# Optimization experiments

Measured on AMD Instinct MI355X. Metric: run time of the kernel, lower is better.

Reference implementation:

```python
import jax, jax.numpy as jnp
import numpy as np

WH, WW = 8, 8
NUM_HEADS = 8
DIM = 256
MLP_HIDDEN = 1024
EPS = 1e-5


def _rel_pos_index(wh, ww):
    ch, cw = np.meshgrid(np.arange(wh), np.arange(ww), indexing='ij')
    flat = np.stack([ch.ravel(), cw.ravel()])            # (2, N)
    rel = flat[:, :, None] - flat[:, None, :]            # (2, N, N)
    rel = rel.transpose(1, 2, 0).copy()                  # (N, N, 2)
    rel[:, :, 0] += wh - 1
    rel[:, :, 1] += ww - 1
    rel[:, :, 0] *= 2 * ww - 1
    return jnp.asarray(rel.sum(-1))                      # (N, N) int

REL_IDX = _rel_pos_index(WH, WW)


def _layernorm(x, g, b):
    mu = x.mean(-1, keepdims=True)
    var = ((x - mu) ** 2).mean(-1, keepdims=True)
    return (x - mu) * jax.lax.rsqrt(var + EPS) * g + b


def _window_partition(x):
    B, H, W, C = x.shape
    x = x.reshape(B, H // WH, WH, W // WW, WW, C)
    return x.transpose(0, 1, 3, 2, 4, 5).reshape(-1, WH * WW, C)


def _window_reverse(w, B, H, W):
    C = w.shape[-1]
    x = w.reshape(B, H // WH, W // WW, WH, WW, C)
    return x.transpose(0, 1, 3, 2, 4, 5).reshape(B, H, W, C)


def _window_attn(qx, kvx, qw, qb, kvw, kvb, bias_table, pw, pb):
    # qx/kvx: [Bw, N, C]; weights stored as [in, out] (torch Linear transposed)
    Bw, N, C = qx.shape
    hd = C // NUM_HEADS
    scale = hd ** -0.5
    q = (qx @ qw + qb).reshape(Bw, N, NUM_HEADS, hd).transpose(0, 2, 1, 3) * scale
    kv = (kvx @ kvw + kvb).reshape(Bw, N, 2, NUM_HEADS, hd)
    k = kv[:, :, 0].transpose(0, 2, 1, 3)
    v = kv[:, :, 1].transpose(0, 2, 1, 3)
    attn = jnp.einsum('bhnd,bhmd->bhnm', q, k)
    bias = bias_table[REL_IDX.reshape(-1)].reshape(N, N, NUM_HEADS).transpose(2, 0, 1)
    attn = jax.nn.softmax(attn + bias[None], axis=-1)
    out = jnp.einsum('bhnm,bhmd->bhnd', attn, v).transpose(0, 2, 1, 3).reshape(Bw, N, C)
    return out @ pw + pb


def setup_inputs() -> dict:
    key = jax.random.key(0)
    ks = jax.random.split(key, 16)
    B, H, W, C = 4, 160, 160, DIM
    nW = (H // WH) * (W // WW)
    N = WH * WW
    n_bias = (2 * WH - 1) * (2 * WW - 1)  # 225
    s = 0.02
    return {
        'x': jax.random.normal(ks[0], (B, H, W, C), jnp.float32),
        'enc_feat': jax.random.normal(ks[1], (B, H, W, C), jnp.float32),
        'mask_matrix': jnp.zeros((nW, N, N), jnp.float32),
        'norm1_g': jnp.ones((C,), jnp.float32),
        'norm1_b': jnp.zeros((C,), jnp.float32),
        'q1_w': jax.random.normal(ks[2], (C, C), jnp.float32) * s,
        'q1_b': jnp.zeros((C,), jnp.float32),
        'kv1_w': jax.random.normal(ks[3], (C, 2 * C), jnp.float32) * s,
        'kv1_b': jnp.zeros((2 * C,), jnp.float32),
        'bias1': jax.random.normal(ks[4], (n_bias, NUM_HEADS), jnp.float32) * s,
        'proj1_w': jax.random.normal(ks[5], (C, C), jnp.float32) * s,
        'proj1_b': jnp.zeros((C,), jnp.float32),
        'q2_w': jax.random.normal(ks[6], (C, C), jnp.float32) * s,
        'q2_b': jnp.zeros((C,), jnp.float32),
        'kv2_w': jax.random.normal(ks[7], (C, 2 * C), jnp.float32) * s,
        'kv2_b': jnp.zeros((2 * C,), jnp.float32),
        'bias2': jax.random.normal(ks[8], (n_bias, NUM_HEADS), jnp.float32) * s,
        'proj2_w': jax.random.normal(ks[9], (C, C), jnp.float32) * s,
        'proj2_b': jnp.zeros((C,), jnp.float32),
        'norm2_g': jnp.ones((C,), jnp.float32),
        'norm2_b': jnp.zeros((C,), jnp.float32),
        'fc1_w': jax.random.normal(ks[10], (C, MLP_HIDDEN), jnp.float32) * s,
        'fc1_b': jnp.zeros((MLP_HIDDEN,), jnp.float32),
        'fc2_w': jax.random.normal(ks[11], (MLP_HIDDEN, C), jnp.float32) * s,
        'fc2_b': jnp.zeros((C,), jnp.float32),
    }


def reference(x, enc_feat, mask_matrix, norm1_g, norm1_b, q1_w, q1_b, kv1_w, kv1_b,
              bias1, proj1_w, proj1_b, q2_w, q2_b, kv2_w, kv2_b, bias2, proj2_w,
              proj2_b, norm2_g, norm2_b, fc1_w, fc1_b, fc2_w, fc2_b):
    # NOTE: the source forward never passes mask_matrix into attention; faithful here.
    B, H, W, C = x.shape
    shortcut = x
    xn = _layernorm(x, norm1_g, norm1_b)
    xw = _window_partition(xn)              # [B*nW, N, C]
    ew = _window_partition(enc_feat)        # [B*nW, N, C]
    # windowed self-attention with relative position bias
    xw = _window_attn(xw, xw, q1_w, q1_b, kv1_w, kv1_b, bias1, proj1_w, proj1_b)
    # windowed cross-attention to encoder features
    xw = _window_attn(xw, ew, q2_w, q2_b, kv2_w, kv2_b, bias2, proj2_w, proj2_b)
    x = shortcut + _window_reverse(xw, B, H, W)
    h = _layernorm(x, norm2_g, norm2_b)
    h = jax.nn.gelu(h @ fc1_w + fc1_b, approximate=False) @ fc2_w + fc2_b
    return x + h
```

## Files before the change

### kernel.cpp

```cpp
#include <hip/hip_runtime.h>

typedef __attribute__((ext_vector_type(4))) float f32x4;
typedef __attribute__((ext_vector_type(8))) short bf16x8;
typedef __attribute__((ext_vector_type(8))) unsigned short ushort8;
typedef unsigned short u16;
typedef unsigned int u32;

#define LDS_AS(p) ((__attribute__((address_space(3))) void*)(p))
#define GLB_AS(p) ((const __attribute__((address_space(1))) void*)(p))

__device__ __forceinline__ u16 f2b(float f) {
    u32 u = __builtin_bit_cast(u32, f);
    u32 r = (u + 0x7fffu + ((u >> 16) & 1u)) >> 16;
    return (u16)r;
}

__device__ __forceinline__ void vmwait(int n) {
    if (n == 0)
        asm volatile("s_waitcnt vmcnt(0)" ::: "memory");
    else if (n == 4)
        asm volatile("s_waitcnt vmcnt(4)" ::: "memory");
    else if (n == 8)
        asm volatile("s_waitcnt vmcnt(8)" ::: "memory");
    else
        asm volatile("s_waitcnt vmcnt(12)" ::: "memory");
}

struct PrepAll {
    const float* src[8];
    u16* dst[8];
    int K[8];
    int N[8];
    float S[8];
};

__global__ __launch_bounds__(256) void prep_w(PrepAll p) {
    const int wi = blockIdx.y;
    const int K = p.K[wi], N = p.N[wi];
    const int e = blockIdx.x * 256 + threadIdx.x;
    if (e >= K * N) return;
    const int k = e / N, n = e % N;
    p.dst[wi][n * K + k] = f2b(p.src[wi][e] * p.S[wi]);
}

__global__ __launch_bounds__(64) void prep_bias(const float* __restrict__ t1,
                                                const float* __restrict__ t2,
                                                float* __restrict__ Bm) {
    const int j = threadIdx.x;
    const int i = blockIdx.x;
    const int hh = blockIdx.y;
    const int s = hh >> 3, h = hh & 7;
    const int idx = ((i >> 3) - (j >> 3) + 7) * 15 + ((i & 7) - (j & 7) + 7);
    const float* tab = s ? t2 : t1;
    Bm[(long)hh * 4096 + i * 64 + j] = tab[idx * 8 + h];
}

__global__ __launch_bounds__(256) void prep_bcat(const float* __restrict__ q1b,
                                                 const float* __restrict__ kv1b,
                                                 const float* __restrict__ q2b,
                                                 float qs, float* __restrict__ b1cat,
                                                 float* __restrict__ q2bs) {
    const int g = blockIdx.x * 256 + threadIdx.x;
    if (g < 256) {
        b1cat[g] = qs * q1b[g];
        q2bs[g] = qs * q2b[g];
    } else if (g < 768) {
        b1cat[g] = kv1b[g - 256];
    }
}

__global__ __launch_bounds__(256) void cast_bf(const float* __restrict__ in,
                                               u16* __restrict__ out) {
    const long i = (long)blockIdx.x * 256 + threadIdx.x;
    const float4 a = *(const float4*)(in + i * 8);
    const float4 b = *(const float4*)(in + i * 8 + 4);
    ushort8 o;
    o[0] = f2b(a.x); o[1] = f2b(a.y); o[2] = f2b(a.z); o[3] = f2b(a.w);
    o[4] = f2b(b.x); o[5] = f2b(b.y); o[6] = f2b(b.z); o[7] = f2b(b.w);
    *(ushort8*)(out + i * 8) = o;
}

__global__ __launch_bounds__(256) void ln256(const float* __restrict__ x,
                                             const float* __restrict__ g,
                                             const float* __restrict__ b,
                                             u16* __restrict__ out) {
    const int lane = threadIdx.x & 63;
    const long row = (long)blockIdx.x * 4 + (threadIdx.x >> 6);
    const float4 v = *(const float4*)(x + row * 256 + lane * 4);
    float s = v.x + v.y + v.z + v.w;
    float s2 = v.x * v.x + v.y * v.y + v.z * v.z + v.w * v.w;
#pragma unroll
    for (int off = 32; off > 0; off >>= 1) {
        s += __shfl_xor(s, off);
        s2 += __shfl_xor(s2, off);
    }
    const float mu = s * (1.f / 256.f);
    const float var = s2 * (1.f / 256.f) - mu * mu;
    const float rr = rsqrtf(var + 1e-5f);
    const int c = lane * 4;
    const float4 gv = *(const float4*)(g + c);
    const float4 bv = *(const float4*)(b + c);
    ushort4 o;
    o.x = f2b((v.x - mu) * rr * gv.x + bv.x);
    o.y = f2b((v.y - mu) * rr * gv.y + bv.y);
    o.z = f2b((v.z - mu) * rr * gv.z + bv.z);
    o.w = f2b((v.w - mu) * rr * gv.w + bv.w);
    *(ushort4*)(out + row * 256 + c) = o;
}

template <int EPI, int NT>
__global__ __launch_bounds__(256, 2) void gemmQ(const u16* __restrict__ A,
                                                const u16* __restrict__ Bt,
                                                const float* __restrict__ bias,
                                                const float* __restrict__ res,
                                                u16* outb, float* outf,
                                                int N, int Nt) {
    constexpr int K = NT * 32;
    static_assert(NT >= 4, "pipeline needs >= 4 K-tiles");
    __shared__ u16 lds[4][2][128 * 32];
    const int t = threadIdx.x;
    const int lane = t & 63;
    const int wave = t >> 6;
    const int wr = wave >> 1, wc = wave & 1;
    const int l15 = lane & 15, lg = lane >> 4;

    const int per = gridDim.x >> 3;
    const int id2 = (blockIdx.x & 7) * per + (blockIdx.x >> 3);
    const int bm = id2 / Nt, bn = id2 % Nt;
    const long m0 = (long)bm * 128;
    const int n0 = bn * 128;

    const u16* Ag = A + (m0 + (t >> 2)) * K + (t & 3) * 8;
    const u16* Bg = Bt + (long)(n0 + (t >> 2)) * K + (t & 3) * 8;

    auto stage = [&](int tile) {
        const int b = tile & 3;
        const int k0 = tile * 32;
        u16* Al = lds[b][0] + t * 8;
        u16* Bl = lds[b][1] + t * 8;
        __builtin_amdgcn_global_load_lds(GLB_AS(Ag + k0), LDS_AS(Al), 16, 0, 0);
        __builtin_amdgcn_global_load_lds(GLB_AS(Ag + (long)64 * K + k0), LDS_AS(Al + 2048), 16, 0, 0);
        __builtin_amdgcn_global_load_lds(GLB_AS(Bg + k0), LDS_AS(Bl), 16, 0, 0);
        __builtin_amdgcn_global_load_lds(GLB_AS(Bg + (long)64 * K + k0), LDS_AS(Bl + 2048), 16, 0, 0);
    };

    f32x4 acc[4][4];
#pragma unroll
    for (int i = 0; i < 4; i++)
#pragma unroll
        for (int j = 0; j < 4; j++) acc[i][j] = (f32x4){0.f, 0.f, 0.f, 0.f};

    stage(0);
    stage(1);
    stage(2);
    stage(3);

#pragma unroll
    for (int tt = 0; tt < NT; ++tt) {
        const int cur = tt & 3;
        const int rem = NT - 1 - tt;
        vmwait(4 * (rem > 3 ? 3 : rem));
        __builtin_amdgcn_s_barrier();

        bf16x8 af[4], bfr[4];
#pragma unroll
        for (int i = 0; i < 4; i++)
            af[i] = *(const bf16x8*)(lds[cur][0] + (wr * 64 + i * 16 + l15) * 32 + lg * 8);
#pragma unroll
        for (int i = 0; i < 4; i++)
            bfr[i] = *(const bf16x8*)(lds[cur][1] + (wc * 64 + i * 16 + l15) * 32 + lg * 8);
        asm volatile("s_waitcnt lgkmcnt(0)" ::: "memory");
        __builtin_amdgcn_sched_barrier(0);
        __builtin_amdgcn_s_barrier();

        if (tt + 4 < NT) stage(tt + 4);

#pragma unroll
        for (int mi = 0; mi < 4; mi++)
#pragma unroll
            for (int ni = 0; ni < 4; ni++)
                acc[mi][ni] = __builtin_amdgcn_mfma_f32_16x16x32_bf16(af[mi], bfr[ni], acc[mi][ni], 0, 0, 0);
    }

#pragma unroll
    for (int mi = 0; mi < 4; mi++) {
#pragma unroll
        for (int ni = 0; ni < 4; ni++) {
            const int col = n0 + wc * 64 + ni * 16 + l15;
            const float bv = bias[col];
#pragma unroll
            for (int r = 0; r < 4; r++) {
                const long row = m0 + wr * 64 + mi * 16 + lg * 4 + r;
                float v = acc[mi][ni][r] + bv;
                if (EPI == 2) v = 0.5f * v * (1.f + erff(v * 0.70710678118f));
                const long idx = row * N + col;
                if (EPI == 3)
                    outf[idx] = v + res[idx];
                else
                    outb[idx] = f2b(v);
            }
        }
    }
}

__global__ __launch_bounds__(256) void attn64(const u16* __restrict__ Q, int qs,
                                              const u16* __restrict__ KV, int ks,
                                              const float* __restrict__ Bm,
                                              u16* __restrict__ AO) {
    __shared__ u16 Plds[4][64 * 72];
    __shared__ u16 Vt[4][32 * 72];
    const int lane = threadIdx.x & 63, wave = threadIdx.x >> 6;
    const int wh = blockIdx.x * 4 + wave;
    const int w = wh >> 3, h = wh & 7;
    const int b = w / 400, rem = w % 400;
    const int wy = rem / 20, wx = rem % 20;
    const long base_t = (long)b * 25600 + wy * 8 * 160 + wx * 8;
    const int l15 = lane & 15, lg = lane >> 4;

    bf16x8 qf[4], kf[4];
#pragma unroll
    for (int ti = 0; ti < 4; ti++) {
        const int r = ti * 16 + l15;
        const long tt = base_t + (r >> 3) * 160 + (r & 7);
        qf[ti] = *(const bf16x8*)(Q + tt * qs + h * 32 + lg * 8);
        kf[ti] = *(const bf16x8*)(KV + tt * ks + h * 32 + lg * 8);
    }
    const f32x4 zz = (f32x4){0.f, 0.f, 0.f, 0.f};
    f32x4 s[4][4];
#pragma unroll
    for (int ti = 0; ti < 4; ti++)
#pragma unroll
        for (int tj = 0; tj < 4; tj++)
            s[ti][tj] = __builtin_amdgcn_mfma_f32_16x16x32_bf16(qf[ti], kf[tj], zz, 0, 0, 0);

    {
        const long tt = base_t + (lane >> 3) * 160 + (lane & 7);
        const u16* vrow = KV + tt * ks + 256 + h * 32;
#pragma unroll
        for (int cg = 0; cg < 4; cg++) {
            bf16x8 v8 = *(const bf16x8*)(vrow + cg * 8);
#pragma unroll
            for (int j = 0; j < 8; j++) Vt[wave][(cg * 8 + j) * 72 + lane] = (u16)v8[j];
        }
    }

    const float* Bh = Bm + h * 4096;
#pragma unroll
    for (int ti = 0; ti < 4; ti++) {
#pragma unroll
        for (int r = 0; r < 4; r++) {
            const int i = ti * 16 + lg * 4 + r;
            float vv[4];
            float m = -1e30f;
#pragma unroll
            for (int tj = 0; tj < 4; tj++) {
                vv[tj] = s[ti][tj][r] + Bh[i * 64 + tj * 16 + l15];
                m = fmaxf(m, vv[tj]);
            }
#pragma unroll
            for (int off = 1; off < 16; off <<= 1) m = fmaxf(m, __shfl_xor(m, off));
            float sum = 0.f;
#pragma unroll
            for (int tj = 0; tj < 4; tj++) {
                vv[tj] = __expf(vv[tj] - m);
                sum += vv[tj];
            }
#pragma unroll
            for (int off = 1; off < 16; off <<= 1) sum += __shfl_xor(sum, off);
            const float inv = 1.f / sum;
#pragma unroll
            for (int tj = 0; tj < 4; tj++)
                Plds[wave][i * 72 + tj * 16 + l15] = f2b(vv[tj] * inv);
        }
    }

    f32x4 o[4][2];
#pragma unroll
    for (int mi = 0; mi < 4; mi++)
#pragma unroll
        for (int n = 0; n < 2; n++) o[mi][n] = zz;
#pragma unroll
    for (int c = 0; c < 2; c++) {
        bf16x8 vf[2];
#pragma unroll
        for (int n = 0; n < 2; n++)
            vf[n] = *(const bf16x8*)(&Vt[wave][(n * 16 + l15) * 72 + c * 32 + lg * 8]);
#pragma unroll
        for (int mi = 0; mi < 4; mi++) {
            bf16x8 pf = *(const bf16x8*)(&Plds[wave][(mi * 16 + l15) * 72 + c * 32 + lg * 8]);
#pragma unroll
            for (int n = 0; n < 2; n++)
                o[mi][n] = __builtin_amdgcn_mfma_f32_16x16x32_bf16(pf, vf[n], o[mi][n], 0, 0, 0);
        }
    }
#pragma unroll
    for (int mi = 0; mi < 4; mi++) {
#pragma unroll
        for (int n = 0; n < 2; n++) {
#pragma unroll
            for (int r = 0; r < 4; r++) {
                const int i = mi * 16 + lg * 4 + r;
                const long tt = base_t + (i >> 3) * 160 + (i & 7);
                AO[tt * 256 + h * 32 + n * 16 + l15] = f2b(o[mi][n][r]);
            }
        }
    }
}

extern "C" void kernel_launch(void* const* d_in, const int* in_sizes, int n_in,
                              void* d_out, int out_size, void* d_ws, size_t ws_size,
                              hipStream_t stream) {
    const float* x    = (const float*)d_in[0];
    const float* enc  = (const float*)d_in[1];
    const float* n1g  = (const float*)d_in[3];
    const float* n1b  = (const float*)d_in[4];
    const float* q1w  = (const float*)d_in[5];
    const float* q1b  = (const float*)d_in[6];
    const float* kv1w = (const float*)d_in[7];
    const float* kv1b = (const float*)d_in[8];
    const float* bias1 = (const float*)d_in[9];
    const float* p1w  = (const float*)d_in[10];
    const float* p1b  = (const float*)d_in[11];
    const float* q2w  = (const float*)d_in[12];
    const float* q2b  = (const float*)d_in[13];
    const float* kv2w = (const float*)d_in[14];
    const float* kv2b = (const float*)d_in[15];
    const float* bias2 = (const float*)d_in[16];
    const float* p2w  = (const float*)d_in[17];
    const float* p2b  = (const float*)d_in[18];
    const float* n2g  = (const float*)d_in[19];
    const float* n2b  = (const float*)d_in[20];
    const float* f1w  = (const float*)d_in[21];
    const float* f1b  = (const float*)d_in[22];
    const float* f2w  = (const float*)d_in[23];
    const float* f2bias = (const float*)d_in[24];
    float* out = (float*)d_out;

    char* ws = (char*)d_ws;
    size_t off = 0;
    auto alloc = [&](size_t bytes) {
        char* p = ws + off;
        off += (bytes + 255) & ~(size_t)255;
        return p;
    };
    u16* Wt    = (u16*)alloc(1048576 * 2);
    float* Bm  = (float*)alloc(16 * 4096 * 4);
    float* b1c = (float*)alloc(768 * 4);
    float* q2s = (float*)alloc(256 * 4);
    u16* xn    = (u16*)alloc(52428800);
    u16* qb    = (u16*)alloc(52428800);
    u16* kvb   = (u16*)alloc(104857600);
    u16* ao    = (u16*)alloc(52428800);
    u16* encb  = (u16*)alloc(52428800);

    u16* qkv = qb;
    u16* h1  = kvb;

    u16 *q1t = Wt, *p1t = Wt + 196608, *q2t = Wt + 262144,
        *kv2t = Wt + 327680, *p2t = Wt + 458752, *f1t = Wt + 524288, *f2t = Wt + 786432;

    const float qscale = 0.17677669529663687f;

    PrepAll pa;
    pa.src[0] = q1w;  pa.dst[0] = q1t;        pa.K[0] = 256;  pa.N[0] = 256;  pa.S[0] = qscale;
    pa.src[1] = kv1w; pa.dst[1] = Wt + 65536; pa.K[1] = 256;  pa.N[1] = 512;  pa.S[1] = 1.f;
    pa.src[2] = p1w;  pa.dst[2] = p1t;        pa.K[2] = 256;  pa.N[2] = 256;  pa.S[2] = 1.f;
    pa.src[3] = q2w;  pa.dst[3] = q2t;        pa.K[3] = 256;  pa.N[3] = 256;  pa.S[3] = qscale;
    pa.src[4] = kv2w; pa.dst[4] = kv2t;       pa.K[4] = 256;  pa.N[4] = 512;  pa.S[4] = 1.f;
    pa.src[5] = p2w;  pa.dst[5] = p2t;        pa.K[5] = 256;  pa.N[5] = 256;  pa.S[5] = 1.f;
    pa.src[6] = f1w;  pa.dst[6] = f1t;        pa.K[6] = 256;  pa.N[6] = 1024; pa.S[6] = 1.f;
    pa.src[7] = f2w;  pa.dst[7] = f2t;        pa.K[7] = 1024; pa.N[7] = 256;  pa.S[7] = 1.f;
    prep_w<<<dim3(1024, 8), 256, 0, stream>>>(pa);
    prep_bias<<<dim3(64, 16), 64, 0, stream>>>(bias1, bias2, Bm);
    prep_bcat<<<dim3(3), 256, 0, stream>>>(q1b, kv1b, q2b, qscale, b1c, q2s);
    cast_bf<<<dim3(12800), 256, 0, stream>>>(enc, encb);
    ln256<<<dim3(25600), 256, 0, stream>>>(x, n1g, n1b, xn);

    gemmQ<0, 8><<<dim3(4800), 256, 0, stream>>>(xn, q1t, b1c, nullptr, qkv, nullptr, 768, 6);
    attn64<<<dim3(3200), 256, 0, stream>>>(qkv, 768, qkv + 256, 768, Bm, ao);
    gemmQ<0, 8><<<dim3(1600), 256, 0, stream>>>(ao, p1t, p1b, nullptr, xn, nullptr, 256, 2);

    gemmQ<0, 8><<<dim3(1600), 256, 0, stream>>>(xn, q2t, q2s, nullptr, qb, nullptr, 256, 2);
    gemmQ<0, 8><<<dim3(3200), 256, 0, stream>>>(encb, kv2t, kv2b, nullptr, kvb, nullptr, 512, 4);
    attn64<<<dim3(3200), 256, 0, stream>>>(qb, 256, kvb, 512, Bm + 8 * 4096, ao);

    gemmQ<3, 8><<<dim3(1600), 256, 0, stream>>>(ao, p2t, p2b, x, (u16*)nullptr, out, 256, 2);

    ln256<<<dim3(25600), 256, 0, stream>>>(out, n2g, n2b, qb);
    for (int c = 0; c < 2; c++) {
        const u16* xh = qb + (size_t)c * 51200 * 256;
        float* oc = out + (size_t)c * 51200 * 256;
        gemmQ<2, 8><<<dim3(3200), 256, 0, stream>>>(xh, f1t, f1b, nullptr, h1, nullptr, 1024, 8);
        gemmQ<3, 32><<<dim3(800), 256, 0, stream>>>(h1, f2t, f2bias, oc, (u16*)nullptr, oc, 256, 2);
    }
}
```

Baseline: 890.0 us.

## Add weight-stationary GEMM for K=256 projections and fuse residual with LayerNorm

Adds a `bres` GEMM kernel for the K=256 GEMMs (QKV, both proj layers, q2, kv2 and fc1). Each wave keeps its 64-column slice of the weight in registers and streams 256 rows of activations through swizzled, double-buffered LDS; the fc1 version applies GELU in the epilogue. The second projection now writes bf16, and a new `ln_add` kernel does the residual add and the second LayerNorm in one pass. The MLP is no longer split into two chunks, and the elementwise and prep kernels loop over several rows or grid-stride to cut block counts. The aim is to reuse each weight tile across many rows and to remove extra launches and fp32 round trips. In exchange, register pressure goes up, the proj2 output is rounded to bf16 before the residual add, and the full-size hidden buffer now runs past `kvb` into the `ao`/`encb` workspace, which is dead by that point.

```diff
diff --git a/kernel.cpp b/kernel.cpp
--- a/kernel.cpp
+++ b/kernel.cpp
@@ -13,6 +13,9 @@
     u32 u = __builtin_bit_cast(u32, f);
     u32 r = (u + 0x7fffu + ((u >> 16) & 1u)) >> 16;
     return (u16)r;
+}
+__device__ __forceinline__ float b2f(u16 u) {
+    return __builtin_bit_cast(float, (u32)u << 16);
 }
 
 __device__ __forceinline__ void vmwait(int n) {
@@ -37,22 +40,23 @@
 __global__ __launch_bounds__(256) void prep_w(PrepAll p) {
     const int wi = blockIdx.y;
     const int K = p.K[wi], N = p.N[wi];
-    const int e = blockIdx.x * 256 + threadIdx.x;
-    if (e >= K * N) return;
-    const int k = e / N, n = e % N;
-    p.dst[wi][n * K + k] = f2b(p.src[wi][e] * p.S[wi]);
-}
-
-__global__ __launch_bounds__(64) void prep_bias(const float* __restrict__ t1,
-                                                const float* __restrict__ t2,
-                                                float* __restrict__ Bm) {
-    const int j = threadIdx.x;
-    const int i = blockIdx.x;
-    const int hh = blockIdx.y;
+    for (int e = blockIdx.x * 256 + threadIdx.x; e < K * N; e += gridDim.x * 256) {
+        const int k = e / N, n = e % N;
+        p.dst[wi][n * K + k] = f2b(p.src[wi][e] * p.S[wi]);
+    }
+}
+
+__global__ __launch_bounds__(256) void prep_bias(const float* __restrict__ t1,
+                                                 const float* __restrict__ t2,
+                                                 float* __restrict__ Bm) {
+    const int hh = blockIdx.x;
     const int s = hh >> 3, h = hh & 7;
-    const int idx = ((i >> 3) - (j >> 3) + 7) * 15 + ((i & 7) - (j & 7) + 7);
     const float* tab = s ? t2 : t1;
-    Bm[(long)hh * 4096 + i * 64 + j] = tab[idx * 8 + h];
+    const int j = threadIdx.x & 63;
+    for (int i = threadIdx.x >> 6; i < 64; i += 4) {
+        const int idx = ((i >> 3) - (j >> 3) + 7) * 15 + ((i & 7) - (j & 7) + 7);
+        Bm[(long)hh * 4096 + i * 64 + j] = tab[idx * 8 + h];
+    }
 }
 
 __global__ __launch_bounds__(256) void prep_bcat(const float* __restrict__ q1b,
@@ -70,14 +74,15 @@
 }
 
 __global__ __launch_bounds__(256) void cast_bf(const float* __restrict__ in,
-                                               u16* __restrict__ out) {
-    const long i = (long)blockIdx.x * 256 + threadIdx.x;
-    const float4 a = *(const float4*)(in + i * 8);
-    const float4 b = *(const float4*)(in + i * 8 + 4);
-    ushort8 o;
-    o[0] = f2b(a.x); o[1] = f2b(a.y); o[2] = f2b(a.z); o[3] = f2b(a.w);
-    o[4] = f2b(b.x); o[5] = f2b(b.y); o[6] = f2b(b.z); o[7] = f2b(b.w);
-    *(ushort8*)(out + i * 8) = o;
+                                               u16* __restrict__ out, long n8) {
+    for (long i = (long)blockIdx.x * 256 + threadIdx.x; i < n8; i += (long)gridDim.x * 256) {
+        const float4 a = *(const float4*)(in + i * 8);
+        const float4 b = *(const float4*)(in + i * 8 + 4);
+        ushort8 o;
+        o[0] = f2b(a.x); o[1] = f2b(a.y); o[2] = f2b(a.z); o[3] = f2b(a.w);
+        o[4] = f2b(b.x); o[5] = f2b(b.y); o[6] = f2b(b.z); o[7] = f2b(b.w);
+        *(ushort8*)(out + i * 8) = o;
+    }
 }
 
 __global__ __launch_bounds__(256) void ln256(const float* __restrict__ x,
@@ -85,27 +90,152 @@
                                              const float* __restrict__ b,
                                              u16* __restrict__ out) {
     const int lane = threadIdx.x & 63;
-    const long row = (long)blockIdx.x * 4 + (threadIdx.x >> 6);
-    const float4 v = *(const float4*)(x + row * 256 + lane * 4);
-    float s = v.x + v.y + v.z + v.w;
-    float s2 = v.x * v.x + v.y * v.y + v.z * v.z + v.w * v.w;
-#pragma unroll
-    for (int off = 32; off > 0; off >>= 1) {
-        s += __shfl_xor(s, off);
-        s2 += __shfl_xor(s2, off);
-    }
-    const float mu = s * (1.f / 256.f);
-    const float var = s2 * (1.f / 256.f) - mu * mu;
-    const float rr = rsqrtf(var + 1e-5f);
     const int c = lane * 4;
     const float4 gv = *(const float4*)(g + c);
     const float4 bv = *(const float4*)(b + c);
-    ushort4 o;
-    o.x = f2b((v.x - mu) * rr * gv.x + bv.x);
-    o.y = f2b((v.y - mu) * rr * gv.y + bv.y);
-    o.z = f2b((v.z - mu) * rr * gv.z + bv.z);
-    o.w = f2b((v.w - mu) * rr * gv.w + bv.w);
-    *(ushort4*)(out + row * 256 + c) = o;
+#pragma unroll
+    for (int it = 0; it < 8; ++it) {
+        const long row = (long)blockIdx.x * 32 + it * 4 + (threadIdx.x >> 6);
+        const float4 v = *(const float4*)(x + row * 256 + c);
+        float s = v.x + v.y + v.z + v.w;
+        float s2 = v.x * v.x + v.y * v.y + v.z * v.z + v.w * v.w;
+#pragma unroll
+        for (int off = 32; off > 0; off >>= 1) {
+            s += __shfl_xor(s, off);
+            s2 += __shfl_xor(s2, off);
+        }
+        const float mu = s * (1.f / 256.f);
+        const float rr = rsqrtf(s2 * (1.f / 256.f) - mu * mu + 1e-5f);
+        ushort4 o;
+        o.x = f2b((v.x - mu) * rr * gv.x + bv.x);
+        o.y = f2b((v.y - mu) * rr * gv.y + bv.y);
+        o.z = f2b((v.z - mu) * rr * gv.z + bv.z);
+        o.w = f2b((v.w - mu) * rr * gv.w + bv.w);
+        *(ushort4*)(out + row * 256 + c) = o;
+    }
+}
+
+__global__ __launch_bounds__(256) void ln_add(const float* __restrict__ x,
+                                              const u16* __restrict__ p,
+                                              const float* __restrict__ g,
+                                              const float* __restrict__ b,
+                                              float* __restrict__ out,
+                                              u16* __restrict__ xo) {
+    const int lane = threadIdx.x & 63;
+    const int c = lane * 4;
+    const float4 gv = *(const float4*)(g + c);
+    const float4 bv = *(const float4*)(b + c);
+#pragma unroll
+    for (int it = 0; it < 8; ++it) {
+        const long row = (long)blockIdx.x * 32 + it * 4 + (threadIdx.x >> 6);
+        float4 v = *(const float4*)(x + row * 256 + c);
+        const ushort4 pb = *(const ushort4*)(p + row * 256 + c);
+        v.x += b2f(pb.x); v.y += b2f(pb.y); v.z += b2f(pb.z); v.w += b2f(pb.w);
+        *(float4*)(out + row * 256 + c) = v;
+        float s = v.x + v.y + v.z + v.w;
+        float s2 = v.x * v.x + v.y * v.y + v.z * v.z + v.w * v.w;
+#pragma unroll
+        for (int off = 32; off > 0; off >>= 1) {
+            s += __shfl_xor(s, off);
+            s2 += __shfl_xor(s2, off);
+        }
+        const float mu = s * (1.f / 256.f);
+        const float rr = rsqrtf(s2 * (1.f / 256.f) - mu * mu + 1e-5f);
+        ushort4 o;
+        o.x = f2b((v.x - mu) * rr * gv.x + bv.x);
+        o.y = f2b((v.y - mu) * rr * gv.y + bv.y);
+        o.z = f2b((v.z - mu) * rr * gv.z + bv.z);
+        o.w = f2b((v.w - mu) * rr * gv.w + bv.w);
+        *(ushort4*)(xo + row * 256 + c) = o;
+    }
+}
+
+template <int EPI, int NGRP>
+__global__ __launch_bounds__(256, 2) void bres(const u16* __restrict__ A,
+                                               const u16* __restrict__ Bt,
+                                               const float* __restrict__ bias,
+                                               u16* __restrict__ outb) {
+    constexpr int N = NGRP * 256;
+    __shared__ u16 lds[2][8192];
+    const int t = threadIdx.x, lane = t & 63, wave = t >> 6;
+    const int l15 = lane & 15, lg = lane >> 4;
+
+    const int per = gridDim.x >> 3;
+    const int id2 = (blockIdx.x & 7) * per + (blockIdx.x >> 3);
+    const int mb = id2 / NGRP, ng = id2 % NGRP;
+    const long m0 = (long)mb * 256;
+    const int ncol0 = ng * 256 + wave * 64;
+
+    float bcol[4];
+#pragma unroll
+    for (int n = 0; n < 4; n++) bcol[n] = bias[ncol0 + n * 16 + l15];
+
+    bf16x8 bset[8][4];
+#pragma unroll
+    for (int k = 0; k < 8; k++)
+#pragma unroll
+        for (int n = 0; n < 4; n++)
+            bset[k][n] = *(const bf16x8*)(Bt + (long)(ncol0 + n * 16 + l15) * 256 + k * 32 + lg * 8);
+
+    const int srow = t >> 5, schunk = t & 31;
+    auto stage = [&](int ms, int buf) {
+        const u16* src = A + (m0 + ms * 32) * 256;
+#pragma unroll
+        for (int j = 0; j < 4; j++) {
+            const int row = j * 8 + srow;
+            const int chunk = schunk ^ (row & 7);
+            __builtin_amdgcn_global_load_lds(GLB_AS(src + row * 256 + chunk * 8),
+                                             LDS_AS(&lds[buf][(j * 256 + t) * 8]), 16, 0, 0);
+        }
+    };
+
+    f32x4 acc[2][4];
+#pragma unroll
+    for (int mi = 0; mi < 2; mi++)
+#pragma unroll
+        for (int n = 0; n < 4; n++) acc[mi][n] = (f32x4){0.f, 0.f, 0.f, 0.f};
+
+    stage(0, 0);
+    stage(1, 1);
+
+#pragma unroll
+    for (int ms = 0; ms < 8; ++ms) {
+        if (ms < 7) vmwait(4);
+        else        vmwait(0);
+        __builtin_amdgcn_s_barrier();
+        const int buf = ms & 1;
+#pragma unroll
+        for (int s = 0; s < 8; s++) {
+            bf16x8 af[2];
+#pragma unroll
+            for (int mi = 0; mi < 2; mi++)
+                af[mi] = *(const bf16x8*)&lds[buf][(mi * 16 + l15) * 256 +
+                                                   (((s * 4 + lg) ^ (l15 & 7)) * 8)];
+#pragma unroll
+            for (int mi = 0; mi < 2; mi++)
+#pragma unroll
+                for (int n = 0; n < 4; n++)
+                    acc[mi][n] = __builtin_amdgcn_mfma_f32_16x16x32_bf16(af[mi], bset[s][n], acc[mi][n], 0, 0, 0);
+        }
+        asm volatile("s_waitcnt lgkmcnt(0)" ::: "memory");
+        __builtin_amdgcn_s_barrier();
+
+#pragma unroll
+        for (int mi = 0; mi < 2; mi++) {
+#pragma unroll
+            for (int n = 0; n < 4; n++) {
+#pragma unroll
+                for (int r = 0; r < 4; r++) {
+                    float v = acc[mi][n][r] + bcol[n];
+                    if (EPI == 2) v = 0.5f * v * (1.f + erff(v * 0.70710678118f));
+                    const long row = m0 + ms * 32 + mi * 16 + lg * 4 + r;
+                    outb[row * N + ncol0 + n * 16 + l15] = f2b(v);
+                }
+                acc[mi][n] = (f32x4){0.f, 0.f, 0.f, 0.f};
+            }
+        }
+        if (ms + 2 < 8) stage(ms + 2, buf);
+    }
 }
 
 template <int EPI, int NT>
@@ -116,7 +246,6 @@
                                                 u16* outb, float* outf,
                                                 int N, int Nt) {
     constexpr int K = NT * 32;
-    static_assert(NT >= 4, "pipeline needs >= 4 K-tiles");
     __shared__ u16 lds[4][2][128 * 32];
     const int t = threadIdx.x;
     const int lane = t & 63;
@@ -150,10 +279,7 @@
 #pragma unroll
         for (int j = 0; j < 4; j++) acc[i][j] = (f32x4){0.f, 0.f, 0.f, 0.f};
 
-    stage(0);
-    stage(1);
-    stage(2);
-    stage(3);
+    stage(0); stage(1); stage(2); stage(3);
 
 #pragma unroll
     for (int tt = 0; tt < NT; ++tt) {
@@ -327,7 +453,7 @@
     const float* kv2b = (const float*)d_in[15];
     const float* bias2 = (const float*)d_in[16];
     const float* p2w  = (const float*)d_in[17];
-    const float* p2b  = (const float*)d_in[18];
+    const float* p2bi = (const float*)d_in[18];
     const float* n2g  = (const float*)d_in[19];
     const float* n2b  = (const float*)d_in[20];
     const float* f1w  = (const float*)d_in[21];
@@ -355,6 +481,7 @@
 
     u16* qkv = qb;
     u16* h1  = kvb;
+    u16* pj2 = xn;
 
     u16 *q1t = Wt, *p1t = Wt + 196608, *q2t = Wt + 262144,
         *kv2t = Wt + 327680, *p2t = Wt + 458752, *f1t = Wt + 524288, *f2t = Wt + 786432;
@@ -370,27 +497,23 @@
     pa.src[5] = p2w;  pa.dst[5] = p2t;        pa.K[5] = 256;  pa.N[5] = 256;  pa.S[5] = 1.f;
     pa.src[6] = f1w;  pa.dst[6] = f1t;        pa.K[6] = 256;  pa.N[6] = 1024; pa.S[6] = 1.f;
     pa.src[7] = f2w;  pa.dst[7] = f2t;        pa.K[7] = 1024; pa.N[7] = 256;  pa.S[7] = 1.f;
-    prep_w<<<dim3(1024, 8), 256, 0, stream>>>(pa);
-    prep_bias<<<dim3(64, 16), 64, 0, stream>>>(bias1, bias2, Bm);
+    prep_w<<<dim3(128, 8), 256, 0, stream>>>(pa);
+    prep_bias<<<dim3(16), 256, 0, stream>>>(bias1, bias2, Bm);
     prep_bcat<<<dim3(3), 256, 0, stream>>>(q1b, kv1b, q2b, qscale, b1c, q2s);
-    cast_bf<<<dim3(12800), 256, 0, stream>>>(enc, encb);
-    ln256<<<dim3(25600), 256, 0, stream>>>(x, n1g, n1b, xn);
-
-    gemmQ<0, 8><<<dim3(4800), 256, 0, stream>>>(xn, q1t, b1c, nullptr, qkv, nullptr, 768, 6);
+    cast_bf<<<dim3(2048), 256, 0, stream>>>(enc, encb, 3276800);
+    ln256<<<dim3(3200), 256, 0, stream>>>(x, n1g, n1b, xn);
+
+    bres<0, 3><<<dim3(1200), 256, 0, stream>>>(xn, q1t, b1c, qkv);
     attn64<<<dim3(3200), 256, 0, stream>>>(qkv, 768, qkv + 256, 768, Bm, ao);
-    gemmQ<0, 8><<<dim3(1600), 256, 0, stream>>>(ao, p1t, p1b, nullptr, xn, nullptr, 256, 2);
-
-    gemmQ<0, 8><<<dim3(1600), 256, 0, stream>>>(xn, q2t, q2s, nullptr, qb, nullptr, 256, 2);
-    gemmQ<0, 8><<<dim3(3200), 256, 0, stream>>>(encb, kv2t, kv2b, nullptr, kvb, nullptr, 512, 4);
+    bres<0, 1><<<dim3(400), 256, 0, stream>>>(ao, p1t, p1b, xn);
+
+    bres<0, 1><<<dim3(400), 256, 0, stream>>>(xn, q2t, q2s, qb);
+    bres<0, 2><<<dim3(800), 256, 0, stream>>>(encb, kv2t, kv2b, kvb);
     attn64<<<dim3(3200), 256, 0, stream>>>(qb, 256, kvb, 512, Bm + 8 * 4096, ao);
 
-    gemmQ<3, 8><<<dim3(1600), 256, 0, stream>>>(ao, p2t, p2b, x, (u16*)nullptr, out, 256, 2);
-
-    ln256<<<dim3(25600), 256, 0, stream>>>(out, n2g, n2b, qb);
-    for (int c = 0; c < 2; c++) {
-        const u16* xh = qb + (size_t)c * 51200 * 256;
-        float* oc = out + (size_t)c * 51200 * 256;
-        gemmQ<2, 8><<<dim3(3200), 256, 0, stream>>>(xh, f1t, f1b, nullptr, h1, nullptr, 1024, 8);
-        gemmQ<3, 32><<<dim3(800), 256, 0, stream>>>(h1, f2t, f2bias, oc, (u16*)nullptr, oc, 256, 2);
-    }
-}
+    bres<0, 1><<<dim3(400), 256, 0, stream>>>(ao, p2t, p2bi, pj2);
+    ln_add<<<dim3(3200), 256, 0, stream>>>(x, pj2, n2g, n2b, out, qb);
+
+    bres<2, 4><<<dim3(1600), 256, 0, stream>>>(qb, f1t, f1b, h1);
+    gemmQ<3, 32><<<dim3(1600), 256, 0, stream>>>(h1, f2t, f2bias, out, (u16*)nullptr, out, 256, 2);
+}
```

Result: slower. 1.266 ms (+42.3%).
